# Kernel optimization log

Hardware: AMD Instinct MI355X
Metric: run time of the kernel (lower is better)

## Reference

```python
import jax, jax.numpy as jnp
import numpy as np

N_NODES = 100000
N_EDGES = 3200000
IN_CH = 128
HID = 32


def setup_inputs() -> dict:
    key = jax.random.key(0)
    ks = jax.random.split(key, 8)
    x = jax.random.normal(ks[0], (N_NODES, IN_CH), dtype=jnp.float32)
    edge_index = jax.random.randint(ks[1], (2, N_EDGES), 0, N_NODES, dtype=jnp.int64)
    # Glorot-ish scaled weights
    W1 = jax.random.normal(ks[2], (IN_CH, HID), dtype=jnp.float32) / np.sqrt(IN_CH)
    b1 = jnp.zeros((HID,), dtype=jnp.float32)
    W2 = jax.random.normal(ks[3], (HID, HID), dtype=jnp.float32) / np.sqrt(HID)
    b2 = jnp.zeros((HID,), dtype=jnp.float32)
    Wc = jax.random.normal(ks[4], (HID, 2), dtype=jnp.float32) / np.sqrt(HID)
    bc = jnp.zeros((2,), dtype=jnp.float32)
    return {"x": x, "edge_index": edge_index, "W1": W1, "b1": b1,
            "W2": W2, "b2": b2, "Wc": Wc, "bc": bc}


def _gcn_norm(edge_index, n_nodes):
    # PyG GCNConv default: add self-loops, symmetric normalization
    src, dst = edge_index[0], edge_index[1]
    loops = jnp.arange(n_nodes, dtype=src.dtype)
    src = jnp.concatenate([src, loops])
    dst = jnp.concatenate([dst, loops])
    deg = jax.ops.segment_sum(jnp.ones_like(dst, dtype=jnp.float32), dst,
                              num_segments=n_nodes)
    dis = jnp.where(deg > 0, jax.lax.rsqrt(deg), 0.0)  # deg^{-1/2}
    norm = dis[src] * dis[dst]                          # [E + N]
    return src, dst, norm


def _gcn_conv(x, W, b, src, dst, norm, n_nodes):
    h = x @ W                                   # [N, out] linear first (out <= in)
    msg = h[src] * norm[:, None]                # gather + scale  [E+N, out]
    out = jax.ops.segment_sum(msg, dst, num_segments=n_nodes)  # scatter-add
    return out + b


def reference(x, edge_index, W1, b1, W2, b2, Wc, bc):
    n = x.shape[0]
    src, dst, norm = _gcn_norm(edge_index, n)
    h = jax.nn.relu(_gcn_conv(x, W1, b1, src, dst, norm, n))
    h = jax.nn.relu(_gcn_conv(h, W2, b2, src, dst, norm, n))
    return h @ Wc + bc                          # [N, 2]
```

## Files before the change

### kernel.cpp

```cpp
#include <hip/hip_runtime.h>

#define NCH 32
#define INCH 128
#define SH 7
#define BNODES 128
#define CAP 4544
#define P1_CHUNK 4096
#define NBINS_PAD 1024
#define HB 8

typedef float  f4 __attribute__((ext_vector_type(4)));
typedef unsigned int u32;
typedef u32    uv4 __attribute__((ext_vector_type(4)));

__device__ __forceinline__ u32 pack_bf16x2(float a, float b) {
  u32 ua = __float_as_uint(a);
  u32 ub = __float_as_uint(b);
  ua = (ua + 0x7FFFu + ((ua >> 16) & 1u)) >> 16;
  ub = (ub + 0x7FFFu + ((ub >> 16) & 1u)) & 0xFFFF0000u;
  return ub | ua;
}
__device__ __forceinline__ float lo_bf16(u32 u) { return __uint_as_float(u << 16); }
__device__ __forceinline__ float hi_bf16(u32 u) { return __uint_as_float(u & 0xFFFF0000u); }

__global__ void k_initcur(int* gcur, int nbk) {
  int i = blockIdx.x * blockDim.x + threadIdx.x;
  if (i < nbk) gcur[i] = i * CAP;
}

__global__ __launch_bounds__(256) void k_part(const int* __restrict__ ei, int* gcur,
                                              u32* __restrict__ srcsb, int E) {
  __shared__ u32 sorted[P1_CHUNK];
  __shared__ unsigned short aux[P1_CHUNK];
  __shared__ int hist[NBINS_PAD];
  __shared__ int bbase[NBINS_PAD + 1];
  __shared__ int bfill[NBINS_PAD];
  __shared__ int wsums[4];
  const int tid = threadIdx.x;
  const int base = blockIdx.x * P1_CHUNK;
  const int cnt = min(P1_CHUNK, E - base);

  for (int i = tid; i < NBINS_PAD; i += 256) hist[i] = 0;
  __syncthreads();
  for (int i = tid; i < cnt; i += 256) {
    int d = ei[E + base + i];
    atomicAdd(&hist[d >> SH], 1);
  }
  __syncthreads();
  int c0 = hist[4 * tid], c1 = hist[4 * tid + 1], c2 = hist[4 * tid + 2], c3 = hist[4 * tid + 3];
  int s = c0 + c1 + c2 + c3;
  int lane = tid & 63, w = tid >> 6;
  int incl = s;
#pragma unroll
  for (int off = 1; off < 64; off <<= 1) {
    int t = __shfl_up(incl, off, 64);
    if (lane >= off) incl += t;
  }
  if (lane == 63) wsums[w] = incl;
  __syncthreads();
  int woff = 0;
  for (int i = 0; i < w; ++i) woff += wsums[i];
  int te = woff + incl - s;
  bbase[4 * tid] = te;                     bfill[4 * tid] = te;
  bbase[4 * tid + 1] = te + c0;            bfill[4 * tid + 1] = te + c0;
  bbase[4 * tid + 2] = te + c0 + c1;       bfill[4 * tid + 2] = te + c0 + c1;
  bbase[4 * tid + 3] = te + c0 + c1 + c2;  bfill[4 * tid + 3] = te + c0 + c1 + c2;
  if (tid == 255) bbase[NBINS_PAD] = te + s;
  __syncthreads();
  for (int i = tid; i < cnt; i += 256) {
    int d = ei[E + base + i];
    int srcv = ei[base + i];
    int b = d >> SH;
    int pos = atomicAdd(&bfill[b], 1);
    sorted[pos] = ((u32)(d & (BNODES - 1)) << 17) | (u32)srcv;
    aux[pos] = (unsigned short)b;
  }
  __syncthreads();
  for (int b = tid; b < NBINS_PAD; b += 256) {
    int c = bbase[b + 1] - bbase[b];
    hist[b] = (c > 0) ? atomicAdd(&gcur[b], c) : 0;
  }
  __syncthreads();
  for (int i = tid; i < cnt; i += 256) {
    int b = aux[i];
    int gpos = hist[b] + (i - bbase[b]);
    if (gpos < (b + 1) * CAP) srcsb[gpos] = sorted[i];
  }
}

__global__ __launch_bounds__(256) void k_bsort(const int* __restrict__ gcur,
                                               u32* __restrict__ srcsb,
                                               int2* __restrict__ rowbr,
                                               float* __restrict__ dis, int N) {
  __shared__ u32 raw[CAP];
  __shared__ u32 sbuf[CAP];
  __shared__ int hist2[BNODES];
  __shared__ int fill2[BNODES];
  __shared__ int wsums2[2];
  const int tid = threadIdx.x;
  const int bin = blockIdx.x;
  const int base = bin * CAP;
  int cnt = min(gcur[bin] - base, CAP);

  if (tid < BNODES) hist2[tid] = 0;
  for (int i = tid; i < cnt; i += 256) raw[i] = srcsb[base + i];
  __syncthreads();
  for (int i = tid; i < cnt; i += 256) atomicAdd(&hist2[raw[i] >> 17], 1);
  __syncthreads();
  int deg = (tid < BNODES) ? hist2[tid] : 0;
  int incl = deg;
  {
    int lane = tid & 63;
#pragma unroll
    for (int off = 1; off < 64; off <<= 1) {
      int t = __shfl_up(incl, off, 64);
      if (lane >= off) incl += t;
    }
    if (tid < BNODES && lane == 63) wsums2[tid >> 6] = incl;
  }
  __syncthreads();
  int excl = incl - deg + ((tid >= 64 && tid < BNODES) ? wsums2[0] : 0);
  if (tid < BNODES) fill2[tid] = excl;
  __syncthreads();
  for (int i = tid; i < cnt; i += 256) {
    u32 v = raw[i];
    int pos = atomicAdd(&fill2[v >> 17], 1);
    sbuf[pos] = v & 0x1FFFFu;
  }
  __syncthreads();
  for (int i = tid; i < cnt; i += 256) srcsb[base + i] = sbuf[i];
  if (tid < BNODES) {
    int n = bin * BNODES + tid;
    if (n < N) {
      rowbr[n] = make_int2(base + excl, base + excl + deg);
      dis[n] = rsqrtf((float)(deg + 1));
    }
  }
}

__global__ __launch_bounds__(256) void k_gemm1(const float* __restrict__ x,
                                               const float* __restrict__ W1,
                                               const float* __restrict__ dis,
                                               u32* __restrict__ hsA,
                                               u32* __restrict__ hsB, int N) {
  __shared__ f4 w4[INCH * 8];
  const int tid = threadIdx.x;
  {
    const f4* W14 = (const f4*)W1;
    for (int i = tid; i < INCH * 8; i += 256) w4[i] = W14[i];
  }
  __syncthreads();
  const int cg = tid & 3;
  const int slot = tid >> 2;
  const int nb = blockIdx.x * 128 + slot * 2;
  const int na = min(nb, N - 1);
  const int nb2 = min(nb + 1, N - 1);
  const f4* x4 = (const f4*)x;

  f4 acc0a = (f4)0.f, acc1a = (f4)0.f, acc0b = (f4)0.f, acc1b = (f4)0.f;

#pragma unroll 4
  for (int j = 0; j < 32; ++j) {
    f4 xa = x4[(size_t)na * 32 + j];
    f4 xb = x4[(size_t)nb2 * 32 + j];
#pragma unroll
    for (int r = 0; r < 4; ++r) {
      f4 wA = w4[(4 * j + r) * 8 + cg * 2];
      f4 wB = w4[(4 * j + r) * 8 + cg * 2 + 1];
      acc0a += wA * xa[r];
      acc1a += wB * xa[r];
      acc0b += wA * xb[r];
      acc1b += wB * xb[r];
    }
  }
#pragma unroll
  for (int u = 0; u < 2; ++u) {
    int n = nb + u;
    if (n >= N) break;
    f4 a0 = u ? acc0b : acc0a;
    f4 a1 = u ? acc1b : acc1a;
    float dn = dis[n];
    uv4 o;
    o.x = pack_bf16x2(a0.x * dn, a0.y * dn);
    o.y = pack_bf16x2(a0.z * dn, a0.w * dn);
    o.z = pack_bf16x2(a1.x * dn, a1.y * dn);
    o.w = pack_bf16x2(a1.z * dn, a1.w * dn);
    if (cg < 2) ((uv4*)hsA)[(size_t)n * 2 + cg] = o;
    else        ((uv4*)hsB)[(size_t)n * 2 + (cg - 2)] = o;
  }
}

__device__ __forceinline__ void gather_half(const u32* __restrict__ srcs,
                                            const u32* __restrict__ tbl,
                                            int n, int c, int j, int end,
                                            float& ax, float& ay) {
  u32 su = tbl[(size_t)n * HB + c];
  ax = lo_bf16(su); ay = hi_bf16(su);
  for (; j + 8 <= end; j += 8) {
    u32 u0 = tbl[(size_t)srcs[j] * HB + c];
    u32 u1 = tbl[(size_t)srcs[j + 1] * HB + c];
    u32 u2 = tbl[(size_t)srcs[j + 2] * HB + c];
    u32 u3 = tbl[(size_t)srcs[j + 3] * HB + c];
    u32 u4 = tbl[(size_t)srcs[j + 4] * HB + c];
    u32 u5 = tbl[(size_t)srcs[j + 5] * HB + c];
    u32 u6 = tbl[(size_t)srcs[j + 6] * HB + c];
    u32 u7 = tbl[(size_t)srcs[j + 7] * HB + c];
    ax += ((lo_bf16(u0) + lo_bf16(u1)) + (lo_bf16(u2) + lo_bf16(u3))) +
          ((lo_bf16(u4) + lo_bf16(u5)) + (lo_bf16(u6) + lo_bf16(u7)));
    ay += ((hi_bf16(u0) + hi_bf16(u1)) + (hi_bf16(u2) + hi_bf16(u3))) +
          ((hi_bf16(u4) + hi_bf16(u5)) + (hi_bf16(u6) + hi_bf16(u7)));
  }
  for (; j < end; ++j) {
    u32 u = tbl[(size_t)srcs[j] * HB + c];
    ax += lo_bf16(u);
    ay += hi_bf16(u);
  }
}

__global__ __launch_bounds__(256) void k_aggx(
    const int2* __restrict__ rowbr, const u32* __restrict__ srcs,
    const u32* __restrict__ tblA, const u32* __restrict__ tblB,
    float2* __restrict__ accA, float2* __restrict__ accB, int N) {
  const int half = blockIdx.x & 1;
  int n = (blockIdx.x >> 1) * 32 + (threadIdx.x >> 3);
  int c = threadIdx.x & 7;
  if (n >= N) return;
  const u32* tbl = half ? tblB : tblA;
  float2* acc = half ? accB : accA;
  int2 br = rowbr[n];
  float ax, ay;
  gather_half(srcs, tbl, n, c, br.x, br.y, ax, ay);
  acc[(size_t)n * HB + c] = make_float2(ax, ay);
}

__global__ __launch_bounds__(256) void k_mlp2(
    const float2* __restrict__ accA, const float2* __restrict__ accB,
    const float* __restrict__ dis, const float* __restrict__ b1,
    const float* __restrict__ W2, u32* __restrict__ hs2A,
    u32* __restrict__ hs2B, int N) {
  __shared__ float w[NCH * NCH];
  for (int i = threadIdx.x; i < NCH * NCH; i += blockDim.x) w[i] = W2[i];
  __syncthreads();
  int n = blockIdx.x * 16 + (threadIdx.x >> 4);
  int c2 = threadIdx.x & 15;
  if (n >= N) return;
  float2 a = (c2 < 8) ? accA[(size_t)n * HB + c2] : accB[(size_t)n * HB + (c2 - 8)];
  float dn = dis[n];
  float v0 = fmaxf(fmaf(a.x, dn, b1[2 * c2]), 0.f);
  float v1 = fmaxf(fmaf(a.y, dn, b1[2 * c2 + 1]), 0.f);
  float o0 = 0.f, o1 = 0.f;
#pragma unroll
  for (int k2 = 0; k2 < 16; ++k2) {
    float va = __shfl(v0, k2, 16);
    float vb = __shfl(v1, k2, 16);
    float2 wa = ((const float2*)(w + (2 * k2) * NCH))[c2];
    float2 wb = ((const float2*)(w + (2 * k2 + 1) * NCH))[c2];
    o0 = fmaf(va, wa.x, fmaf(vb, wb.x, o0));
    o1 = fmaf(va, wa.y, fmaf(vb, wb.y, o1));
  }
  u32 p = pack_bf16x2(o0 * dn, o1 * dn);
  if (c2 < 8) hs2A[(size_t)n * HB + c2] = p;
  else        hs2B[(size_t)n * HB + (c2 - 8)] = p;
}

__global__ __launch_bounds__(256) void k_head(
    const float2* __restrict__ accA, const float2* __restrict__ accB,
    const float* __restrict__ dis, const float* __restrict__ b2,
    const float* __restrict__ Wc, const float* __restrict__ bc,
    float* __restrict__ out, int N) {
  int n = blockIdx.x * 16 + (threadIdx.x >> 4);
  int c2 = threadIdx.x & 15;
  if (n >= N) return;
  float2 a = (c2 < 8) ? accA[(size_t)n * HB + c2] : accB[(size_t)n * HB + (c2 - 8)];
  float dn = dis[n];
  float v0 = fmaxf(fmaf(a.x, dn, b2[2 * c2]), 0.f);
  float v1 = fmaxf(fmaf(a.y, dn, b2[2 * c2 + 1]), 0.f);
  float s0 = v0 * Wc[(2 * c2) * 2 + 0] + v1 * Wc[(2 * c2 + 1) * 2 + 0];
  float s1 = v0 * Wc[(2 * c2) * 2 + 1] + v1 * Wc[(2 * c2 + 1) * 2 + 1];
#pragma unroll
  for (int off = 8; off > 0; off >>= 1) {
    s0 += __shfl_down(s0, off, 16);
    s1 += __shfl_down(s1, off, 16);
  }
  if (c2 == 0) {
    out[(size_t)n * 2 + 0] = s0 + bc[0];
    out[(size_t)n * 2 + 1] = s1 + bc[1];
  }
}

extern "C" void kernel_launch(void* const* d_in, const int* in_sizes, int n_in,
                              void* d_out, int out_size, void* d_ws, size_t ws_size,
                              hipStream_t stream) {
  const float* x  = (const float*)d_in[0];
  const int*   ei = (const int*)d_in[1];
  const float* W1 = (const float*)d_in[2];
  const float* b1 = (const float*)d_in[3];
  const float* W2 = (const float*)d_in[4];
  const float* b2 = (const float*)d_in[5];
  const float* Wc = (const float*)d_in[6];
  const float* bc = (const float*)d_in[7];
  float* out = (float*)d_out;

  const int N = in_sizes[0] / INCH;
  const int E = in_sizes[1] / 2;
  const int nbk = (N + BNODES - 1) / BNODES;

  float* dis    = (float*)d_ws;
  int2*  rowbr  = (int2*)(dis + N);
  int*   gcur   = (int*)(rowbr + N);
  u32*   srcsb  = (u32*)(gcur + 784);
  u32*   hsA    = srcsb + (size_t)nbk * CAP;
  u32*   hsB    = hsA + (size_t)N * HB;
  float2* accA  = (float2*)(hsB + (size_t)N * HB);
  float2* accB  = accA + (size_t)N * HB;
  u32*   hs2A   = (u32*)(accB + (size_t)N * HB);
  u32*   hs2B   = hs2A + (size_t)N * HB;

  const int bn = 256;
  const int gP1   = (E + P1_CHUNK - 1) / P1_CHUNK;
  const int gN16  = (N + 15) / 16;
  const int gN32  = (N + 31) / 32;
  const int gN128 = (N + 127) / 128;

  k_initcur<<<(nbk + bn - 1) / bn, bn, 0, stream>>>(gcur, nbk);
  k_part<<<gP1, bn, 0, stream>>>(ei, gcur, srcsb, E);
  k_bsort<<<nbk, bn, 0, stream>>>(gcur, srcsb, rowbr, dis, N);

  k_gemm1<<<gN128, bn, 0, stream>>>(x, W1, dis, hsA, hsB, N);
  k_aggx<<<2 * gN32, bn, 0, stream>>>(rowbr, srcsb, hsA, hsB, accA, accB, N);
  k_mlp2<<<gN16, bn, 0, stream>>>(accA, accB, dis, b1, W2, hs2A, hs2B, N);

  k_aggx<<<2 * gN32, bn, 0, stream>>>(rowbr, srcsb, hs2A, hs2B, accA, accB, N);
  k_head<<<gN16, bn, 0, stream>>>(accA, accB, dis, b2, Wc, bc, out, N);
}
```

Baseline: 194.5 us.

## Aggregate each node with a full wavefront split across edges

The gather-aggregate kernel moves from 8 lanes per node (each lane walking every edge serially) to a full 64-lane wavefront per node. Eight edge slots run in parallel, each with 8 channel lanes, and the partial sums are combined with cross-lane xor shuffles. The goal is more memory-level parallelism and shorter per-thread dependency chains on the random gathers, with an average in-degree around 32. The cost is 8x more blocks, shuffle reduction overhead, and lanes left idle on low-degree nodes.

```diff
diff --git a/kernel.cpp b/kernel.cpp
--- a/kernel.cpp
+++ b/kernel.cpp
@@ -190,47 +190,55 @@
   }
 }
 
-__device__ __forceinline__ void gather_half(const u32* __restrict__ srcs,
-                                            const u32* __restrict__ tbl,
-                                            int n, int c, int j, int end,
-                                            float& ax, float& ay) {
-  u32 su = tbl[(size_t)n * HB + c];
-  ax = lo_bf16(su); ay = hi_bf16(su);
-  for (; j + 8 <= end; j += 8) {
-    u32 u0 = tbl[(size_t)srcs[j] * HB + c];
-    u32 u1 = tbl[(size_t)srcs[j + 1] * HB + c];
-    u32 u2 = tbl[(size_t)srcs[j + 2] * HB + c];
-    u32 u3 = tbl[(size_t)srcs[j + 3] * HB + c];
-    u32 u4 = tbl[(size_t)srcs[j + 4] * HB + c];
-    u32 u5 = tbl[(size_t)srcs[j + 5] * HB + c];
-    u32 u6 = tbl[(size_t)srcs[j + 6] * HB + c];
-    u32 u7 = tbl[(size_t)srcs[j + 7] * HB + c];
-    ax += ((lo_bf16(u0) + lo_bf16(u1)) + (lo_bf16(u2) + lo_bf16(u3))) +
-          ((lo_bf16(u4) + lo_bf16(u5)) + (lo_bf16(u6) + lo_bf16(u7)));
-    ay += ((hi_bf16(u0) + hi_bf16(u1)) + (hi_bf16(u2) + hi_bf16(u3))) +
-          ((hi_bf16(u4) + hi_bf16(u5)) + (hi_bf16(u6) + hi_bf16(u7)));
-  }
-  for (; j < end; ++j) {
-    u32 u = tbl[(size_t)srcs[j] * HB + c];
-    ax += lo_bf16(u);
-    ay += hi_bf16(u);
-  }
-}
-
 __global__ __launch_bounds__(256) void k_aggx(
     const int2* __restrict__ rowbr, const u32* __restrict__ srcs,
     const u32* __restrict__ tblA, const u32* __restrict__ tblB,
     float2* __restrict__ accA, float2* __restrict__ accB, int N) {
   const int half = blockIdx.x & 1;
-  int n = (blockIdx.x >> 1) * 32 + (threadIdx.x >> 3);
-  int c = threadIdx.x & 7;
+  const int wid = threadIdx.x >> 6;
+  const int lane = threadIdx.x & 63;
+  const int es = lane >> 3;
+  const int c = lane & 7;
+  int n = (blockIdx.x >> 1) * 4 + wid;
   if (n >= N) return;
-  const u32* tbl = half ? tblB : tblA;
-  float2* acc = half ? accB : accA;
+  const u32* __restrict__ tbl = half ? tblB : tblA;
+  float2* __restrict__ acc = half ? accB : accA;
   int2 br = rowbr[n];
-  float ax, ay;
-  gather_half(srcs, tbl, n, c, br.x, br.y, ax, ay);
-  acc[(size_t)n * HB + c] = make_float2(ax, ay);
+  int j = br.x;
+  const int end = br.y;
+  float ax = 0.f, ay = 0.f;
+  for (; j + 16 <= end; j += 16) {
+    int s0 = srcs[j + es];
+    int s1 = srcs[j + 8 + es];
+    u32 u0 = tbl[(size_t)s0 * HB + c];
+    u32 u1 = tbl[(size_t)s1 * HB + c];
+    ax += lo_bf16(u0) + lo_bf16(u1);
+    ay += hi_bf16(u0) + hi_bf16(u1);
+  }
+  if (j + 8 <= end) {
+    int s0 = srcs[j + es];
+    u32 u0 = tbl[(size_t)s0 * HB + c];
+    ax += lo_bf16(u0);
+    ay += hi_bf16(u0);
+    j += 8;
+  }
+  if (j + es < end) {
+    int s0 = srcs[j + es];
+    u32 u0 = tbl[(size_t)s0 * HB + c];
+    ax += lo_bf16(u0);
+    ay += hi_bf16(u0);
+  }
+#pragma unroll
+  for (int off = 8; off < 64; off <<= 1) {
+    ax += __shfl_xor(ax, off, 64);
+    ay += __shfl_xor(ay, off, 64);
+  }
+  if (es == 0) {
+    u32 su = tbl[(size_t)n * HB + c];
+    ax += lo_bf16(su);
+    ay += hi_bf16(su);
+    acc[(size_t)n * HB + c] = make_float2(ax, ay);
+  }
 }
 
 __global__ __launch_bounds__(256) void k_mlp2(
@@ -319,17 +327,17 @@
   const int bn = 256;
   const int gP1   = (E + P1_CHUNK - 1) / P1_CHUNK;
   const int gN16  = (N + 15) / 16;
-  const int gN32  = (N + 31) / 32;
   const int gN128 = (N + 127) / 128;
+  const int gAgg  = 2 * ((N + 3) / 4);
 
   k_initcur<<<(nbk + bn - 1) / bn, bn, 0, stream>>>(gcur, nbk);
   k_part<<<gP1, bn, 0, stream>>>(ei, gcur, srcsb, E);
   k_bsort<<<nbk, bn, 0, stream>>>(gcur, srcsb, rowbr, dis, N);
 
   k_gemm1<<<gN128, bn, 0, stream>>>(x, W1, dis, hsA, hsB, N);
-  k_aggx<<<2 * gN32, bn, 0, stream>>>(rowbr, srcsb, hsA, hsB, accA, accB, N);
+  k_aggx<<<gAgg, bn, 0, stream>>>(rowbr, srcsb, hsA, hsB, accA, accB, N);
   k_mlp2<<<gN16, bn, 0, stream>>>(accA, accB, dis, b1, W2, hs2A, hs2B, N);
 
-  k_aggx<<<2 * gN32, bn, 0, stream>>>(rowbr, srcsb, hs2A, hs2B, accA, accB, N);
+  k_aggx<<<gAgg, bn, 0, stream>>>(rowbr, srcsb, hs2A, hs2B, accA, accB, N);
   k_head<<<gN16, bn, 0, stream>>>(accA, accB, dis, b2, Wc, bc, out, N);
 }
```

New measurement: 246.3 us. 1.27x slower.

## Sort nodes by degree within each bin to balance gather wavefronts

Applied to the files above, without the earlier changes.

In k_bsort, each block now counting-sorts its 128 nodes by degree and writes a permutation array. Both aggregation passes then walk nodes in that order, so a wavefront holds nodes of similar degree and lanes diverge less in their loop trip counts. The cost is an extra histogram and scan in the sort kernel, plus one extra indirect load per node in the aggregation. Output writes become scattered within a 128-node window.

```diff
diff --git a/kernel.cpp b/kernel.cpp
--- a/kernel.cpp
+++ b/kernel.cpp
@@ -91,12 +91,15 @@
 __global__ __launch_bounds__(256) void k_bsort(const int* __restrict__ gcur,
                                                u32* __restrict__ srcsb,
                                                int2* __restrict__ rowbr,
-                                               float* __restrict__ dis, int N) {
+                                               float* __restrict__ dis,
+                                               int* __restrict__ perm, int N) {
   __shared__ u32 raw[CAP];
   __shared__ u32 sbuf[CAP];
   __shared__ int hist2[BNODES];
   __shared__ int fill2[BNODES];
+  __shared__ int dfill[BNODES];
   __shared__ int wsums2[2];
+  __shared__ int wsums3[2];
   const int tid = threadIdx.x;
   const int bin = blockIdx.x;
   const int base = bin * CAP;
@@ -121,7 +124,34 @@
   __syncthreads();
   int excl = incl - deg + ((tid >= 64 && tid < BNODES) ? wsums2[0] : 0);
   if (tid < BNODES) fill2[tid] = excl;
-  __syncthreads();
+  const bool validn = (tid < BNODES) && (bin * BNODES + tid < N);
+  const int dc = min(deg, BNODES - 1);
+  if (tid < BNODES) hist2[tid] = 0;
+  __syncthreads();
+  if (validn) atomicAdd(&hist2[dc], 1);
+  __syncthreads();
+  int dv = (tid < BNODES) ? hist2[tid] : 0;
+  int dincl = dv;
+  {
+    int lane = tid & 63;
+#pragma unroll
+    for (int off = 1; off < 64; off <<= 1) {
+      int t = __shfl_up(dincl, off, 64);
+      if (lane >= off) dincl += t;
+    }
+    if (tid < BNODES && lane == 63) wsums3[tid >> 6] = dincl;
+  }
+  __syncthreads();
+  int dexcl = dincl - dv + ((tid >= 64 && tid < BNODES) ? wsums3[0] : 0);
+  if (tid < BNODES) {
+    dfill[tid] = dexcl;
+    perm[bin * BNODES + tid] = -1;
+  }
+  __syncthreads();
+  if (validn) {
+    int r = atomicAdd(&dfill[dc], 1);
+    perm[bin * BNODES + r] = bin * BNODES + tid;
+  }
   for (int i = tid; i < cnt; i += 256) {
     u32 v = raw[i];
     int pos = atomicAdd(&fill2[v >> 17], 1);
@@ -219,14 +249,17 @@
 
 __global__ __launch_bounds__(256) void k_aggx(
     const int2* __restrict__ rowbr, const u32* __restrict__ srcs,
+    const int* __restrict__ perm,
     const u32* __restrict__ tblA, const u32* __restrict__ tblB,
-    float2* __restrict__ accA, float2* __restrict__ accB, int N) {
+    float2* __restrict__ accA, float2* __restrict__ accB, int NP) {
   const int half = blockIdx.x & 1;
-  int n = (blockIdx.x >> 1) * 32 + (threadIdx.x >> 3);
+  int idx = (blockIdx.x >> 1) * 32 + (threadIdx.x >> 3);
   int c = threadIdx.x & 7;
-  if (n >= N) return;
-  const u32* tbl = half ? tblB : tblA;
-  float2* acc = half ? accB : accA;
+  if (idx >= NP) return;
+  int n = perm[idx];
+  if (n < 0) return;
+  const u32* __restrict__ tbl = half ? tblB : tblA;
+  float2* __restrict__ acc = half ? accB : accA;
   int2 br = rowbr[n];
   float ax, ay;
   gather_half(srcs, tbl, n, c, br.x, br.y, ax, ay);
@@ -304,10 +337,12 @@
   const int N = in_sizes[0] / INCH;
   const int E = in_sizes[1] / 2;
   const int nbk = (N + BNODES - 1) / BNODES;
+  const int NP  = nbk * BNODES;
 
   float* dis    = (float*)d_ws;
   int2*  rowbr  = (int2*)(dis + N);
-  int*   gcur   = (int*)(rowbr + N);
+  int*   perm   = (int*)(rowbr + N);
+  int*   gcur   = perm + NP;
   u32*   srcsb  = (u32*)(gcur + 784);
   u32*   hsA    = srcsb + (size_t)nbk * CAP;
   u32*   hsB    = hsA + (size_t)N * HB;
@@ -319,17 +354,17 @@
   const int bn = 256;
   const int gP1   = (E + P1_CHUNK - 1) / P1_CHUNK;
   const int gN16  = (N + 15) / 16;
-  const int gN32  = (N + 31) / 32;
   const int gN128 = (N + 127) / 128;
+  const int gAgg  = 2 * (NP / 32);
 
   k_initcur<<<(nbk + bn - 1) / bn, bn, 0, stream>>>(gcur, nbk);
   k_part<<<gP1, bn, 0, stream>>>(ei, gcur, srcsb, E);
-  k_bsort<<<nbk, bn, 0, stream>>>(gcur, srcsb, rowbr, dis, N);
+  k_bsort<<<nbk, bn, 0, stream>>>(gcur, srcsb, rowbr, dis, perm, N);
 
   k_gemm1<<<gN128, bn, 0, stream>>>(x, W1, dis, hsA, hsB, N);
-  k_aggx<<<2 * gN32, bn, 0, stream>>>(rowbr, srcsb, hsA, hsB, accA, accB, N);
+  k_aggx<<<gAgg, bn, 0, stream>>>(rowbr, srcsb, perm, hsA, hsB, accA, accB, NP);
   k_mlp2<<<gN16, bn, 0, stream>>>(accA, accB, dis, b1, W2, hs2A, hs2B, N);
 
-  k_aggx<<<2 * gN32, bn, 0, stream>>>(rowbr, srcsb, hs2A, hs2B, accA, accB, N);
+  k_aggx<<<gAgg, bn, 0, stream>>>(rowbr, srcsb, perm, hs2A, hs2B, accA, accB, NP);
   k_head<<<gN16, bn, 0, stream>>>(accA, accB, dis, b2, Wc, bc, out, N);
 }
```

Measured after the change: 215.0 us. +10.5%, slower.
